# Performance work log

Measured on AMD Instinct MI355X. Metric: run time of the kernel, lower is better.

The kernel has to match this reference:

```python
import jax, jax.numpy as jnp
import numpy as np

N = 50000
E = 800000
IN_C = 128
OUT_C = 128
N_TYPES = 3
NEG_SLOPE = 0.2  # PyG GATConv default negative_slope


def setup_inputs() -> dict:
    key = jax.random.key(0)
    ks = jax.random.split(key, 10)
    x = jax.random.normal(ks[0], (N, IN_C), dtype=jnp.float32)
    edge_index = jax.random.randint(ks[1], (2, E), 0, N, dtype=jnp.int32)
    edge_type = jax.random.randint(ks[2], (E,), 0, N_TYPES, dtype=jnp.int32)
    node_type = jax.random.randint(ks[3], (N,), 0, 3, dtype=jnp.int32)
    s = 1.0 / np.sqrt(IN_C)
    emb_table = jax.random.normal(ks[4], (3, IN_C), dtype=jnp.float32)
    W = jax.random.normal(ks[5], (N_TYPES, IN_C, OUT_C), dtype=jnp.float32) * s
    att_src = jax.random.normal(ks[6], (N_TYPES, OUT_C), dtype=jnp.float32) * s
    att_dst = jax.random.normal(ks[7], (N_TYPES, OUT_C), dtype=jnp.float32) * s
    bias = jax.random.normal(ks[8], (N_TYPES, OUT_C), dtype=jnp.float32) * 0.01
    return {"x": x, "edge_index": edge_index, "edge_type": edge_type,
            "node_type": node_type, "emb_table": emb_table, "W": W,
            "att_src": att_src, "att_dst": att_dst, "bias": bias}


def reference(x, edge_index, edge_type, node_type, emb_table, W, att_src, att_dst, bias):
    # Eval mode: dropouts are identity. edge_index is non-empty -> GAT branch.
    n = x.shape[0]
    x = x + emb_table[node_type]  # node-type embedding add
    src, dst = edge_index[0], edge_index[1]
    out_sum = jnp.zeros((n, OUT_C), dtype=x.dtype)
    for t in range(N_TYPES):  # per-edge-type GATConv (heads=1, add_self_loops=True)
        xw = x @ W[t]                       # [N, out]
        a_s = xw @ att_src[t]               # [N] alpha_src per node
        a_d = xw @ att_dst[t]               # [N] alpha_dst per node
        mask = edge_type == t               # [E]
        e_raw = jax.nn.leaky_relu(a_s[src] + a_d[dst], NEG_SLOPE)  # [E]
        e_self = jax.nn.leaky_relu(a_s + a_d, NEG_SLOPE)           # [N] self-loop logit
        e_masked = jnp.where(mask, e_raw, -jnp.inf)
        m = jnp.maximum(jax.ops.segment_max(e_masked, dst, num_segments=n), e_self)
        m = jax.lax.stop_gradient(m)
        w_edge = jnp.where(mask, jnp.exp(e_raw - m[dst]), 0.0)     # [E]
        w_self = jnp.exp(e_self - m)                               # [N]
        denom = jax.ops.segment_sum(w_edge, dst, num_segments=n) + w_self
        num = jax.ops.segment_sum(w_edge[:, None] * xw[src], dst, num_segments=n) \
              + w_self[:, None] * xw
        out_sum = out_sum + num / denom[:, None] + bias[t]
        # (attention weights per type are w_edge/denom[dst]; only node output returned)
    return out_sum
```

## Files before the change

kernel.cpp:

```cpp
#include <hip/hip_runtime.h>
#include <math.h>

#define N_NODES 50000
#define N_EDGES 800000
#define C 128
#define NT 3
#define NEG 0.2f
#define CAP 64

#define GEMM_XB 782
#define NCHUNK 782

typedef __attribute__((ext_vector_type(8))) short short8;
typedef __attribute__((ext_vector_type(4))) float f32x4;

__device__ __forceinline__ float leaky(float v) { return v > 0.f ? v : NEG * v; }

__device__ __forceinline__ unsigned short f2bf(float f) {
  unsigned int u = __float_as_uint(f);
  u = (u + 0x7FFFu + ((u >> 16) & 1u)) >> 16;
  return (unsigned short)u;
}
__device__ __forceinline__ float bf_lo(unsigned int w) { return __uint_as_float(w << 16); }
__device__ __forceinline__ float bf_hi(unsigned int w) { return __uint_as_float(w & 0xFFFF0000u); }

__global__ void k_prep(const float* __restrict__ W, unsigned short* __restrict__ Wt,
                       int* __restrict__ cnt) {
  int bid = blockIdx.x;
  if (bid < 192) {
    int idx = bid * 256 + threadIdx.x;
    int t = idx >> 14, rem = idx & 16383;
    int n = rem >> 7, k = rem & 127;
    Wt[((size_t)t * C + n) * C + k] = f2bf(W[((size_t)t * C + k) * C + n]);
  } else {
    int i4 = (bid - 192) * 256 + threadIdx.x;
    if (i4 < N_NODES / 4) ((int4*)cnt)[i4] = make_int4(0, 0, 0, 0);
  }
}

__global__ void k_bm(const float* __restrict__ x, const int* __restrict__ node_type,
                     const float* __restrict__ emb, const unsigned short* __restrict__ Wt,
                     unsigned short* __restrict__ xwb,
                     const float* __restrict__ att_src, const float* __restrict__ att_dst,
                     float* __restrict__ a_s, float2* __restrict__ ad_es,
                     const int* __restrict__ ei, const int* __restrict__ etype,
                     int* __restrict__ cnt, int* __restrict__ buckets) {
  __shared__ unsigned short Bs[128][136];
  const int bid = blockIdx.x;
  const int tid = threadIdx.x;

  if (bid & 1) {
    const int j = bid >> 1;
    const int c = j & 3;
    const int i = j >> 2;
    const int n_c = (c < 2) ? 196 : 195;
    const int dlo = c * 12500, dhi = dlo + 12500;
    for (int cc = i; cc < NCHUNK; cc += n_c) {
      int e0 = cc * 1024 + tid * 4;
      if (e0 + 4 <= N_EDGES) {
        int4 s4 = *(const int4*)(ei + e0);
        int4 d4 = *(const int4*)(ei + N_EDGES + e0);
        int4 t4 = *(const int4*)(etype + e0);
        if (d4.x >= dlo && d4.x < dhi) {
          int p = atomicAdd(&cnt[d4.x], 1);
          if (p < CAP) buckets[(size_t)d4.x * CAP + p] = t4.x * N_NODES + s4.x;
        }
        if (d4.y >= dlo && d4.y < dhi) {
          int p = atomicAdd(&cnt[d4.y], 1);
          if (p < CAP) buckets[(size_t)d4.y * CAP + p] = t4.y * N_NODES + s4.y;
        }
        if (d4.z >= dlo && d4.z < dhi) {
          int p = atomicAdd(&cnt[d4.z], 1);
          if (p < CAP) buckets[(size_t)d4.z * CAP + p] = t4.z * N_NODES + s4.z;
        }
        if (d4.w >= dlo && d4.w < dhi) {
          int p = atomicAdd(&cnt[d4.w], 1);
          if (p < CAP) buckets[(size_t)d4.w * CAP + p] = t4.w * N_NODES + s4.w;
        }
      }
    }
    return;
  }

  const int rb = bid >> 1;
  const int wid = tid >> 6, lane = tid & 63;
  const int m = lane & 15, quad = lane >> 4;
  const int row0 = rb * 64;

  short8 af[4];
  {
    int arow = row0 + wid * 16 + m;
    bool valid = arow < N_NODES;
    const float* xr = x + (size_t)(valid ? arow : 0) * C;
    int nt = valid ? node_type[arow] : 0;
    const float* er = emb + nt * C;
#pragma unroll
    for (int k0i = 0; k0i < 4; ++k0i) {
      int cb = k0i * 32 + quad * 8;
      float4 v0 = *(const float4*)(xr + cb);
      float4 v1 = *(const float4*)(xr + cb + 4);
      float4 e0 = *(const float4*)(er + cb);
      float4 e1 = *(const float4*)(er + cb + 4);
      short8 f;
      f[0] = (short)f2bf(v0.x + e0.x);
      f[1] = (short)f2bf(v0.y + e0.y);
      f[2] = (short)f2bf(v0.z + e0.z);
      f[3] = (short)f2bf(v0.w + e0.w);
      f[4] = (short)f2bf(v1.x + e1.x);
      f[5] = (short)f2bf(v1.y + e1.y);
      f[6] = (short)f2bf(v1.z + e1.z);
      f[7] = (short)f2bf(v1.w + e1.w);
      af[k0i] = f;
    }
  }

#pragma unroll
  for (int it = 0; it < 8; ++it) {
    int c = tid + it * 256;
    int n = c >> 4, kc = c & 15;
    *(uint4*)&Bs[n][kc * 8] = *(const uint4*)(Wt + (size_t)n * C + kc * 8);
  }
  __syncthreads();

  for (int t = 0; t < NT; ++t) {
    f32x4 acc[8] = {};
#pragma unroll
    for (int k0i = 0; k0i < 4; ++k0i) {
      int k0 = k0i * 32;
#pragma unroll
      for (int j = 0; j < 8; ++j) {
        short8 b = *(const short8*)&Bs[j * 16 + m][k0 + quad * 8];
        acc[j] = __builtin_amdgcn_mfma_f32_16x16x32_bf16(af[k0i], b, acc[j], 0, 0, 0);
      }
    }

    float ps[4] = {}, pd[4] = {};
#pragma unroll
    for (int j = 0; j < 8; ++j) {
      float as = att_src[t * C + j * 16 + m];
      float ad = att_dst[t * C + j * 16 + m];
#pragma unroll
      for (int reg = 0; reg < 4; ++reg) {
        int row = row0 + wid * 16 + quad * 4 + reg;
        float v = acc[j][reg];
        if (row < N_NODES) xwb[((size_t)t * N_NODES + row) * C + j * 16 + m] = f2bf(v);
        ps[reg] += v * as;
        pd[reg] += v * ad;
      }
    }
#pragma unroll
    for (int off = 1; off < 16; off <<= 1) {
#pragma unroll
      for (int reg = 0; reg < 4; ++reg) {
        ps[reg] += __shfl_xor(ps[reg], off);
        pd[reg] += __shfl_xor(pd[reg], off);
      }
    }
    if (m == 0) {
#pragma unroll
      for (int reg = 0; reg < 4; ++reg) {
        int row = row0 + wid * 16 + quad * 4 + reg;
        if (row < N_NODES) {
          int idx = t * N_NODES + row;
          a_s[idx] = ps[reg];
          ad_es[idx] = make_float2(pd[reg], leaky(ps[reg] + pd[reg]));
        }
      }
    }

    if (t + 1 < NT) {
      __syncthreads();
      const unsigned short* Wtt = Wt + (size_t)(t + 1) * C * C;
#pragma unroll
      for (int it = 0; it < 8; ++it) {
        int c = tid + it * 256;
        int n = c >> 4, kc = c & 15;
        *(uint4*)&Bs[n][kc * 8] = *(const uint4*)(Wtt + (size_t)n * C + kc * 8);
      }
      __syncthreads();
    }
  }
}

__global__ void k_gather(const int* __restrict__ cnt, const int* __restrict__ buckets,
                         const unsigned short* __restrict__ xwb,
                         const float* __restrict__ a_s, const float2* __restrict__ ad_es,
                         const float* __restrict__ bias, float* __restrict__ out) {
  __shared__ float wcs[4][64];
  int wid = threadIdx.x >> 6;
  int lane = threadIdx.x & 63;
  int i = blockIdx.x * 4 + wid;
  int iu = __builtin_amdgcn_readfirstlane(i);
  const int* __restrict__ brow = buckets + (size_t)iu * CAP;
  int n = cnt[iu];
  if (n > CAP) n = CAP;

  int idxl = 0;
  if (lane < n) idxl = brow[lane];
  int tl = idxl >= 2 * N_NODES ? 2 : (idxl >= N_NODES ? 1 : 0);
  float as = a_s[idxl];
  float2 am = ad_es[tl * N_NODES + iu];
  float wl = (lane < n) ? __expf(leaky(as + am.x) - am.y) : 0.f;

  float s0 = tl == 0 ? wl : 0.f;
  float s1 = tl == 1 ? wl : 0.f;
  float s2 = tl == 2 ? wl : 0.f;
#pragma unroll
  for (int off = 1; off < 64; off <<= 1) {
    s0 += __shfl_xor(s0, off);
    s1 += __shfl_xor(s1, off);
    s2 += __shfl_xor(s2, off);
  }
  float inv3[NT] = {1.f / (s0 + 1.f), 1.f / (s1 + 1.f), 1.f / (s2 + 1.f)};
  wcs[wid][lane] = wl * inv3[tl];

  float acc0 = 0.f, acc1 = 0.f;
#pragma unroll
  for (int t = 0; t < NT; ++t) {
    int idx = t * N_NODES + iu;
    float coef = inv3[t];
    unsigned int w = ((const unsigned int*)(xwb + (size_t)idx * C))[lane];
    float2 b2 = ((const float2*)(bias + t * C))[lane];
    acc0 += coef * bf_lo(w) + b2.x;
    acc1 += coef * bf_hi(w) + b2.y;
  }

  const unsigned int* xwu = (const unsigned int*)xwb;
  int j = 0;
  for (; j + 16 <= n; j += 16) {
    float ac0 = 0.f, ac1 = 0.f;
#pragma unroll
    for (int k = 0; k < 16; ++k) {
      int idx = brow[j + k];
      float c = wcs[wid][j + k];
      unsigned int v = xwu[(size_t)idx * (C / 2) + lane];
      ac0 += c * bf_lo(v);
      ac1 += c * bf_hi(v);
    }
    acc0 += ac0; acc1 += ac1;
  }
  for (; j + 8 <= n; j += 8) {
    float ac0 = 0.f, ac1 = 0.f;
#pragma unroll
    for (int k = 0; k < 8; ++k) {
      int idx = brow[j + k];
      float c = wcs[wid][j + k];
      unsigned int v = xwu[(size_t)idx * (C / 2) + lane];
      ac0 += c * bf_lo(v);
      ac1 += c * bf_hi(v);
    }
    acc0 += ac0; acc1 += ac1;
  }
  for (; j < n; ++j) {
    int idx = brow[j];
    float c = wcs[wid][j];
    unsigned int v = xwu[(size_t)idx * (C / 2) + lane];
    acc0 += c * bf_lo(v);
    acc1 += c * bf_hi(v);
  }
  ((float2*)(out + (size_t)iu * C))[lane] = make_float2(acc0, acc1);
}

extern "C" void kernel_launch(void* const* d_in, const int* in_sizes, int n_in,
                              void* d_out, int out_size, void* d_ws, size_t ws_size,
                              hipStream_t stream) {
  const float* x       = (const float*)d_in[0];
  const int* edge_idx  = (const int*)d_in[1];
  const int* edge_type = (const int*)d_in[2];
  const int* node_type = (const int*)d_in[3];
  const float* emb     = (const float*)d_in[4];
  const float* W       = (const float*)d_in[5];
  const float* att_src = (const float*)d_in[6];
  const float* att_dst = (const float*)d_in[7];
  const float* bias    = (const float*)d_in[8];
  float* out = (float*)d_out;

  unsigned short* xwb = (unsigned short*)d_ws;
  unsigned short* Wt  = xwb + (size_t)NT * N_NODES * C;
  float*  a_s   = (float*)(Wt + (size_t)NT * C * C);
  float2* ad_es = (float2*)(a_s + (size_t)NT * N_NODES);
  int*    cnt   = (int*)(ad_es + (size_t)NT * N_NODES);
  int*    buckets = (int*)(cnt + N_NODES);

  k_prep<<<192 + 49, 256, 0, stream>>>(W, Wt, cnt);

  k_bm<<<2 * GEMM_XB, 256, 0, stream>>>(x, node_type, emb, Wt, xwb, att_src, att_dst,
                                        a_s, ad_es, edge_idx, edge_type, cnt, buckets);

  k_gather<<<N_NODES / 4, 256, 0, stream>>>(cnt, buckets, xwb, a_s, ad_es, bias, out);
}
```

Measured before the change: 176.8 us.

## Stage GEMM output through LDS for 16-byte stores and prefetch next W tile

The xw output tile is now staged through per-wave shared memory so each lane writes 16-byte vectors to global memory with nontemporal stores, replacing scattered 2-byte stores. The next edge type's weight tile is prefetched into registers before the MFMA loop so its global load latency overlaps compute. Edge and x input loads use nontemporal hints. This costs extra LDS and register pressure, which may lower occupancy.

Result: slower. 199.6 us (+12.9%).

```diff
diff --git a/kernel.cpp b/kernel.cpp
--- a/kernel.cpp
+++ b/kernel.cpp
@@ -13,6 +13,7 @@
 
 typedef __attribute__((ext_vector_type(8))) short short8;
 typedef __attribute__((ext_vector_type(4))) float f32x4;
+typedef __attribute__((ext_vector_type(4))) int i32x4;
 
 __device__ __forceinline__ float leaky(float v) { return v > 0.f ? v : NEG * v; }
 
@@ -45,7 +46,8 @@
                      float* __restrict__ a_s, float2* __restrict__ ad_es,
                      const int* __restrict__ ei, const int* __restrict__ etype,
                      int* __restrict__ cnt, int* __restrict__ buckets) {
-  __shared__ unsigned short Bs[128][136];
+  __shared__ __align__(16) unsigned short Bs[128][136];
+  __shared__ __align__(16) unsigned short Sc[4][16][136];
   const int bid = blockIdx.x;
   const int tid = threadIdx.x;
 
@@ -58,24 +60,24 @@
     for (int cc = i; cc < NCHUNK; cc += n_c) {
       int e0 = cc * 1024 + tid * 4;
       if (e0 + 4 <= N_EDGES) {
-        int4 s4 = *(const int4*)(ei + e0);
-        int4 d4 = *(const int4*)(ei + N_EDGES + e0);
-        int4 t4 = *(const int4*)(etype + e0);
-        if (d4.x >= dlo && d4.x < dhi) {
-          int p = atomicAdd(&cnt[d4.x], 1);
-          if (p < CAP) buckets[(size_t)d4.x * CAP + p] = t4.x * N_NODES + s4.x;
-        }
-        if (d4.y >= dlo && d4.y < dhi) {
-          int p = atomicAdd(&cnt[d4.y], 1);
-          if (p < CAP) buckets[(size_t)d4.y * CAP + p] = t4.y * N_NODES + s4.y;
-        }
-        if (d4.z >= dlo && d4.z < dhi) {
-          int p = atomicAdd(&cnt[d4.z], 1);
-          if (p < CAP) buckets[(size_t)d4.z * CAP + p] = t4.z * N_NODES + s4.z;
-        }
-        if (d4.w >= dlo && d4.w < dhi) {
-          int p = atomicAdd(&cnt[d4.w], 1);
-          if (p < CAP) buckets[(size_t)d4.w * CAP + p] = t4.w * N_NODES + s4.w;
+        i32x4 s4 = __builtin_nontemporal_load((const i32x4*)(ei + e0));
+        i32x4 d4 = __builtin_nontemporal_load((const i32x4*)(ei + N_EDGES + e0));
+        i32x4 t4 = __builtin_nontemporal_load((const i32x4*)(etype + e0));
+        if (d4[0] >= dlo && d4[0] < dhi) {
+          int p = atomicAdd(&cnt[d4[0]], 1);
+          if (p < CAP) buckets[(size_t)d4[0] * CAP + p] = t4[0] * N_NODES + s4[0];
+        }
+        if (d4[1] >= dlo && d4[1] < dhi) {
+          int p = atomicAdd(&cnt[d4[1]], 1);
+          if (p < CAP) buckets[(size_t)d4[1] * CAP + p] = t4[1] * N_NODES + s4[1];
+        }
+        if (d4[2] >= dlo && d4[2] < dhi) {
+          int p = atomicAdd(&cnt[d4[2]], 1);
+          if (p < CAP) buckets[(size_t)d4[2] * CAP + p] = t4[2] * N_NODES + s4[2];
+        }
+        if (d4[3] >= dlo && d4[3] < dhi) {
+          int p = atomicAdd(&cnt[d4[3]], 1);
+          if (p < CAP) buckets[(size_t)d4[3] * CAP + p] = t4[3] * N_NODES + s4[3];
         }
       }
     }
@@ -97,19 +99,19 @@
 #pragma unroll
     for (int k0i = 0; k0i < 4; ++k0i) {
       int cb = k0i * 32 + quad * 8;
-      float4 v0 = *(const float4*)(xr + cb);
-      float4 v1 = *(const float4*)(xr + cb + 4);
-      float4 e0 = *(const float4*)(er + cb);
-      float4 e1 = *(const float4*)(er + cb + 4);
+      f32x4 v0 = __builtin_nontemporal_load((const f32x4*)(xr + cb));
+      f32x4 v1 = __builtin_nontemporal_load((const f32x4*)(xr + cb + 4));
+      f32x4 e0 = *(const f32x4*)(er + cb);
+      f32x4 e1 = *(const f32x4*)(er + cb + 4);
       short8 f;
-      f[0] = (short)f2bf(v0.x + e0.x);
-      f[1] = (short)f2bf(v0.y + e0.y);
-      f[2] = (short)f2bf(v0.z + e0.z);
-      f[3] = (short)f2bf(v0.w + e0.w);
-      f[4] = (short)f2bf(v1.x + e1.x);
-      f[5] = (short)f2bf(v1.y + e1.y);
-      f[6] = (short)f2bf(v1.z + e1.z);
-      f[7] = (short)f2bf(v1.w + e1.w);
+      f[0] = (short)f2bf(v0[0] + e0[0]);
+      f[1] = (short)f2bf(v0[1] + e0[1]);
+      f[2] = (short)f2bf(v0[2] + e0[2]);
+      f[3] = (short)f2bf(v0[3] + e0[3]);
+      f[4] = (short)f2bf(v1[0] + e1[0]);
+      f[5] = (short)f2bf(v1[1] + e1[1]);
+      f[6] = (short)f2bf(v1[2] + e1[2]);
+      f[7] = (short)f2bf(v1[3] + e1[3]);
       af[k0i] = f;
     }
   }
@@ -118,11 +120,22 @@
   for (int it = 0; it < 8; ++it) {
     int c = tid + it * 256;
     int n = c >> 4, kc = c & 15;
-    *(uint4*)&Bs[n][kc * 8] = *(const uint4*)(Wt + (size_t)n * C + kc * 8);
+    *(i32x4*)&Bs[n][kc * 8] = *(const i32x4*)(Wt + (size_t)n * C + kc * 8);
   }
   __syncthreads();
 
   for (int t = 0; t < NT; ++t) {
+    i32x4 pfr[8];
+    if (t + 1 < NT) {
+      const unsigned short* Wtt = Wt + (size_t)(t + 1) * C * C;
+#pragma unroll
+      for (int it = 0; it < 8; ++it) {
+        int c = tid + it * 256;
+        int n = c >> 4, kc = c & 15;
+        pfr[it] = *(const i32x4*)(Wtt + (size_t)n * C + kc * 8);
+      }
+    }
+
     f32x4 acc[8] = {};
 #pragma unroll
     for (int k0i = 0; k0i < 4; ++k0i) {
@@ -141,9 +154,8 @@
       float ad = att_dst[t * C + j * 16 + m];
 #pragma unroll
       for (int reg = 0; reg < 4; ++reg) {
-        int row = row0 + wid * 16 + quad * 4 + reg;
         float v = acc[j][reg];
-        if (row < N_NODES) xwb[((size_t)t * N_NODES + row) * C + j * 16 + m] = f2bf(v);
+        Sc[wid][quad * 4 + reg][j * 16 + m] = f2bf(v);
         ps[reg] += v * as;
         pd[reg] += v * ad;
       }
@@ -167,15 +179,23 @@
         }
       }
     }
+#pragma unroll
+    for (int p = 0; p < 4; ++p) {
+      int rloc = p * 4 + (lane >> 4);
+      int row = row0 + wid * 16 + rloc;
+      if (row < N_NODES) {
+        i32x4 v = *(const i32x4*)&Sc[wid][rloc][(lane & 15) * 8];
+        __builtin_nontemporal_store(v, (i32x4*)(xwb + ((size_t)t * N_NODES + row) * C + (lane & 15) * 8));
+      }
+    }
 
     if (t + 1 < NT) {
       __syncthreads();
-      const unsigned short* Wtt = Wt + (size_t)(t + 1) * C * C;
 #pragma unroll
       for (int it = 0; it < 8; ++it) {
         int c = tid + it * 256;
         int n = c >> 4, kc = c & 15;
-        *(uint4*)&Bs[n][kc * 8] = *(const uint4*)(Wtt + (size_t)n * C + kc * 8);
+        *(i32x4*)&Bs[n][kc * 8] = pfr[it];
       }
       __syncthreads();
     }
```
